# Kernel tuning notes

Measured on AMD Instinct MI355X. Metric: run time of the kernel, lower is better.

The kernel has to match this reference:

```python
import jax, jax.numpy as jnp
import numpy as np

N, E = 100000, 1600000
F_IN, H, HG, L, C = 128, 128, 128, 3, 40


def setup_inputs() -> dict:
    key = jax.random.key(0)
    ks = jax.random.split(key, 12)
    s = 0.05
    return dict(
        x=jax.random.normal(ks[0], (N, F_IN), jnp.float32),
        edge_index=jax.random.randint(ks[1], (2, E), 0, N),
        edge_weight=jax.random.uniform(ks[2], (E,), jnp.float32),
        h0=jax.random.normal(ks[3], (N, HG), jnp.float32),
        linW=jax.random.normal(ks[4], (F_IN, H), jnp.float32) * s,
        linB=jnp.zeros((H,), jnp.float32),
        convW=jax.random.normal(ks[5], (L, H, H), jnp.float32) * s,
        convB=jnp.zeros((L, H), jnp.float32),
        gru_Wih=jax.random.normal(ks[6], (3 * HG, H), jnp.float32) * s,
        gru_Whh=jax.random.normal(ks[7], (3 * HG, HG), jnp.float32) * s,
        gru_bih=jnp.zeros((3 * HG,), jnp.float32),
        gru_bhh=jnp.zeros((3 * HG,), jnp.float32),
        fcW=jax.random.normal(ks[8], (HG, C), jnp.float32) * s,
        fcB=jnp.zeros((C,), jnp.float32),
    )


def _gru(x, h, Wih, Whh, bih, bhh):
    # torch.nn.GRUCell math (gate order: r, z, n)
    gi = x @ Wih.T + bih  # [N, 3*HG]
    gh = h @ Whh.T + bhh  # [N, 3*HG]
    ir, iz, in_ = jnp.split(gi, 3, axis=-1)
    hr, hz, hn = jnp.split(gh, 3, axis=-1)
    r = jax.nn.sigmoid(ir + hr)
    z = jax.nn.sigmoid(iz + hz)
    n = jnp.tanh(in_ + r * hn)
    return (1.0 - z) * n + z * h


def _gcn_conv(x, src, dst, ew, W, b, n_nodes):
    # PyG GCNConv: linear -> symmetric-normalized sparse aggregation -> bias
    xw = x @ W  # [N, H]
    deg = jax.ops.segment_sum(ew, dst, num_segments=n_nodes)
    dinv = jnp.where(deg > 0, jax.lax.rsqrt(deg), 0.0)
    norm = dinv[src] * ew * dinv[dst]  # [E+N]
    msg = xw[src] * norm[:, None]      # gather + scale (irregular access)
    out = jax.ops.segment_sum(msg, dst, num_segments=n_nodes)  # scatter-add
    return out + b


def reference(x, edge_index, edge_weight, h0, linW, linB, convW, convB,
              gru_Wih, gru_Whh, gru_bih, gru_bhh, fcW, fcB):
    n_nodes = x.shape[0]
    # GCNConv default: add self-loops with weight 1 before normalization
    loops = jnp.arange(n_nodes)
    src = jnp.concatenate([edge_index[0], loops])
    dst = jnp.concatenate([edge_index[1], loops])
    ew = jnp.concatenate([edge_weight, jnp.ones((n_nodes,), edge_weight.dtype)])

    h = h0
    xh = jax.nn.relu(x @ linW + linB)
    h = _gru(xh, h, gru_Wih, gru_Whh, gru_bih, gru_bhh)
    for l in range(convW.shape[0]):  # fixed small layer count
        xh = jax.nn.relu(_gcn_conv(xh, src, dst, ew, convW[l], convB[l], n_nodes))
        h = _gru(xh, h, gru_Wih, gru_Whh, gru_bih, gru_bhh)
    return h @ fcW + fcB
```

## Files before the change

### kernel.cpp

```cpp
#include <hip/hip_runtime.h>
#include <hip/hip_bf16.h>
#include <math.h>

typedef __attribute__((ext_vector_type(8))) short bf8_t;
typedef __attribute__((ext_vector_type(4))) float f4_t;
typedef __attribute__((ext_vector_type(8))) unsigned short us8_t;

__device__ inline unsigned short f2bf(float f) {
  union { float f; unsigned u; } x; x.f = f;
  unsigned r = x.u + 0x7FFF + ((x.u >> 16) & 1);
  return (unsigned short)(r >> 16);
}
__device__ inline float bflo(unsigned v) {
  union { unsigned u; float f; } x; x.u = v << 16; return x.f;
}
__device__ inline float bfhi(unsigned v) {
  union { unsigned u; float f; } x; x.u = v & 0xFFFF0000u; return x.f;
}
__device__ inline float fast_sig(float x) {
  return __builtin_amdgcn_rcpf(1.f + __expf(-x));
}
__device__ inline float fast_tanh(float x) {
  return 1.f - 2.f * __builtin_amdgcn_rcpf(1.f + __expf(2.f * x));
}

__device__ inline void async_copy16(const void* g, void* l) {
  __builtin_amdgcn_global_load_lds(
      (const __attribute__((address_space(1))) unsigned int*)g,
      (__attribute__((address_space(3))) unsigned int*)l, 16, 0, 0);
}


__device__ inline void packB_body(const float* __restrict__ W,
                                  unsigned short* __restrict__ out,
                                  int K, int Ncols, int ldw, int trans, int bid) {
  int idx = bid * 256 + threadIdx.x;
  int total = (Ncols / 16) * (K / 32) * 64;
  if (idx >= total) return;
  int lane = idx & 63;
  int frag = idx >> 6;
  int kt = K / 32;
  int k0 = frag % kt;
  int n0 = frag / kt;
  int n = n0 * 16 + (lane & 15);
  int kbase = k0 * 32 + (lane >> 4) * 8;
  us8_t v;
#pragma unroll
  for (int j = 0; j < 8; ++j) {
    int k = kbase + j;
    float f = trans ? W[(size_t)n * ldw + k] : W[(size_t)k * ldw + n];
    v[j] = f2bf(f);
  }
  *(us8_t*)(out + (size_t)idx * 8) = v;
}

__device__ inline void gemm_body8(const unsigned short* __restrict__ A,
                                  const unsigned short* __restrict__ Bp,
                                  const float* __restrict__ bias,
                                  unsigned short* __restrict__ C, int M, int bid,
                                  bool relu, bool hasbias, unsigned char* smem) {
  int wave = threadIdx.x >> 6, lane = threadIdx.x & 63;
  int row0 = (bid * 8 + wave) * 16;
  int m = lane & 15, q = lane >> 4;

#pragma unroll
  for (int i = 0; i < 4; ++i) {
    int f = wave * 4 + i;
    async_copy16((const unsigned char*)Bp + (size_t)f * 1024 + lane * 16,
                 smem + f * 1024);
  }
  __syncthreads();
  if (row0 >= M) return;

  int arow = row0 + m; if (arow >= M) arow = M - 1;
  bf8_t a[4];
#pragma unroll
  for (int k0 = 0; k0 < 4; ++k0)
    a[k0] = *(const bf8_t*)(A + (size_t)arow * 128 + k0 * 32 + q * 8);

#pragma unroll
  for (int n0 = 0; n0 < 8; ++n0) {
    f4_t acc = {};
#pragma unroll
    for (int k0 = 0; k0 < 4; ++k0) {
      bf8_t b = *(const bf8_t*)(smem + (n0 * 4 + k0) * 1024 + lane * 16);
      acc = __builtin_amdgcn_mfma_f32_16x16x32_bf16(a[k0], b, acc, 0, 0, 0);
    }
    int col = n0 * 16 + m;
    float bs = hasbias ? bias[col] : 0.f;
#pragma unroll
    for (int r = 0; r < 4; ++r) {
      int grow = row0 + q * 4 + r;
      if (grow < M) {
        float v = acc[r] + bs;
        if (relu) v = fmaxf(v, 0.f);
        C[(size_t)grow * 128 + col] = f2bf(v);
      }
    }
  }
}

__device__ inline void gru_stage8(const unsigned short* __restrict__ Bi,
                                  const unsigned short* __restrict__ Bh,
                                  unsigned char* smem, int wave, int lane, int g) {
#pragma unroll
  for (int i = 0; i < 3; ++i) {
    int f = wave * 3 + i;
    int s = f >> 2, k0 = f & 3;
    int cc = g + 8 * (s >= 3 ? s - 3 : s);
    const unsigned short* src = (s < 3) ? Bi : Bh;
    async_copy16((const unsigned char*)src + ((size_t)(cc * 4 + k0)) * 1024 + lane * 16,
                 smem + f * 1024);
  }
}

__device__ inline void gru_core(const bf8_t* ax, const float* h_in, float* h_out,
                                const unsigned short* __restrict__ Bi,
                                const unsigned short* __restrict__ Bh,
                                const float* __restrict__ bih, const float* __restrict__ bhh,
                                int M, int row0, int wave, int lane, unsigned char* smem) {
  int m = lane & 15, q = lane >> 4;
  int arow = row0 + m; if (arow >= M) arow = M - 1;

  bf8_t ah[4];
#pragma unroll
  for (int k0 = 0; k0 < 4; ++k0) {
    const float* hp = h_in + (size_t)arow * 128 + k0 * 32 + q * 8;
    float4 h0 = *(const float4*)hp;
    float4 h1 = *(const float4*)(hp + 4);
    bf8_t t;
    t[0] = (short)f2bf(h0.x); t[1] = (short)f2bf(h0.y);
    t[2] = (short)f2bf(h0.z); t[3] = (short)f2bf(h0.w);
    t[4] = (short)f2bf(h1.x); t[5] = (short)f2bf(h1.y);
    t[6] = (short)f2bf(h1.z); t[7] = (short)f2bf(h1.w);
    ah[k0] = t;
  }

  int erow[4];
#pragma unroll
  for (int r = 0; r < 4; ++r) {
    int gr = row0 + q * 4 + r;
    erow[r] = (gr < M) ? gr : (M - 1);
  }

  float hp_cur[4], hp_nxt[4];
#pragma unroll
  for (int r = 0; r < 4; ++r)
    hp_cur[r] = h_in[(size_t)erow[r] * 128 + m];

#pragma unroll
  for (int g = 0; g < 8; ++g) {
    __syncthreads();
    f4_t air = {}, aiz = {}, ain = {}, ahr = {}, ahz = {}, ahn = {};
#pragma unroll
    for (int k0 = 0; k0 < 4; ++k0) {
      bf8_t br = *(const bf8_t*)(smem + (0 * 4 + k0) * 1024 + lane * 16);
      bf8_t bz = *(const bf8_t*)(smem + (1 * 4 + k0) * 1024 + lane * 16);
      bf8_t bn = *(const bf8_t*)(smem + (2 * 4 + k0) * 1024 + lane * 16);
      bf8_t cr = *(const bf8_t*)(smem + (3 * 4 + k0) * 1024 + lane * 16);
      bf8_t cz = *(const bf8_t*)(smem + (4 * 4 + k0) * 1024 + lane * 16);
      bf8_t cn = *(const bf8_t*)(smem + (5 * 4 + k0) * 1024 + lane * 16);
      air = __builtin_amdgcn_mfma_f32_16x16x32_bf16(ax[k0], br, air, 0, 0, 0);
      aiz = __builtin_amdgcn_mfma_f32_16x16x32_bf16(ax[k0], bz, aiz, 0, 0, 0);
      ain = __builtin_amdgcn_mfma_f32_16x16x32_bf16(ax[k0], bn, ain, 0, 0, 0);
      ahr = __builtin_amdgcn_mfma_f32_16x16x32_bf16(ah[k0], cr, ahr, 0, 0, 0);
      ahz = __builtin_amdgcn_mfma_f32_16x16x32_bf16(ah[k0], cz, ahz, 0, 0, 0);
      ahn = __builtin_amdgcn_mfma_f32_16x16x32_bf16(ah[k0], cn, ahn, 0, 0, 0);
    }
    if (g < 7) {
#pragma unroll
      for (int r = 0; r < 4; ++r)
        hp_nxt[r] = h_in[(size_t)erow[r] * 128 + (g + 1) * 16 + m];
    }
    __syncthreads();
    if (g < 7) gru_stage8(Bi, Bh, smem, wave, lane, g + 1);

    int col = g * 16 + m;
    float bir_ = bih[col], biz_ = bih[col + 128], bin_ = bih[col + 256];
    float bhr_ = bhh[col], bhz_ = bhh[col + 128], bhn_ = bhh[col + 256];
#pragma unroll
    for (int r = 0; r < 4; ++r) {
      int grow = row0 + q * 4 + r;
      if (grow < M) {
        float rr = fast_sig(air[r] + bir_ + ahr[r] + bhr_);
        float zz = fast_sig(aiz[r] + biz_ + ahz[r] + bhz_);
        float nn = fast_tanh(ain[r] + bin_ + rr * (ahn[r] + bhn_));
        h_out[(size_t)grow * 128 + col] = (1.f - zz) * nn + zz * hp_cur[r];
      }
    }
#pragma unroll
    for (int r = 0; r < 4; ++r) hp_cur[r] = hp_nxt[r];
  }
}


__global__ __launch_bounds__(256) void k_prep(
    const float* __restrict__ linW, const float* __restrict__ convW,
    const float* __restrict__ Wih, const float* __restrict__ Whh,
    unsigned short* __restrict__ linWp, unsigned short* __restrict__ convWp,
    unsigned short* __restrict__ Bi, unsigned short* __restrict__ Bh,
    int* __restrict__ cnt, int N) {
  int b = blockIdx.x;
  if (b < 8)  { packB_body(linW, linWp, 128, 128, 128, 0, b); return; }
  if (b < 32) { int l = (b - 8) >> 3;
                packB_body(convW + (size_t)l * 16384, convWp + (size_t)l * 16384,
                           128, 128, 128, 0, (b - 8) & 7); return; }
  if (b < 56) { packB_body(Wih, Bi, 128, 384, 128, 1, b - 32); return; }
  if (b < 80) { packB_body(Whh, Bh, 128, 384, 128, 1, b - 56); return; }
  int i = (b - 80) * 256 + threadIdx.x;
  if (i < N) cnt[i] = 0;
}

__global__ __launch_bounds__(256) void k_count_f2bf(
    const int* __restrict__ dst, int* __restrict__ cnt, int* __restrict__ pos, int E,
    const float* __restrict__ xin, unsigned short* __restrict__ xout, size_t n8,
    int nCnt) {
  if ((int)blockIdx.x < nCnt) {
    int e = blockIdx.x * 256 + threadIdx.x;
    if (e < E) pos[e] = atomicAdd(&cnt[dst[e]], 1);
    return;
  }
  size_t i = (size_t)(blockIdx.x - nCnt) * 256 + threadIdx.x;
  if (i >= n8) return;
  const float4* p = (const float4*)(xin + i * 8);
  float4 a = p[0], b = p[1];
  us8_t v;
  v[0] = f2bf(a.x); v[1] = f2bf(a.y); v[2] = f2bf(a.z); v[3] = f2bf(a.w);
  v[4] = f2bf(b.x); v[5] = f2bf(b.y); v[6] = f2bf(b.z); v[7] = f2bf(b.w);
  *(us8_t*)(xout + i * 8) = v;
}

__global__ __launch_bounds__(256) void k_scan_block(
    const int* __restrict__ cnt, int* __restrict__ partial,
    int* __restrict__ bsum, int n) {
  __shared__ int s[256];
  int tid = threadIdx.x;
  int i = blockIdx.x * 256 + tid;
  s[tid] = (i < n) ? cnt[i] : 0;
  __syncthreads();
#pragma unroll
  for (int d = 1; d < 256; d <<= 1) {
    int t = (tid >= d) ? s[tid - d] : 0;
    __syncthreads();
    s[tid] += t;
    __syncthreads();
  }
  if (i < n) partial[i] = s[tid];
  if (tid == 255) bsum[blockIdx.x] = s[255];
}

__global__ __launch_bounds__(512) void k_scan_sums(int* __restrict__ bsum, int nb) {
  __shared__ int s[512];
  int tid = threadIdx.x;
  s[tid] = (tid < nb) ? bsum[tid] : 0;
  __syncthreads();
#pragma unroll
  for (int d = 1; d < 512; d <<= 1) {
    int t = (tid >= d) ? s[tid - d] : 0;
    __syncthreads();
    s[tid] += t;
    __syncthreads();
  }
  if (tid < nb) bsum[tid] = s[tid];
}

__global__ __launch_bounds__(256) void k_scan_add(
    const int* __restrict__ partial, const int* __restrict__ bsum,
    int* __restrict__ rowptr, int n) {
  int i = blockIdx.x * 256 + threadIdx.x;
  if (i == 0) rowptr[0] = 0;
  if (i < n) {
    int v = partial[i] + (blockIdx.x > 0 ? bsum[blockIdx.x - 1] : 0);
    rowptr[i + 1] = v;
  }
}

__global__ __launch_bounds__(512) void k_fill(
    const int* __restrict__ src, const int* __restrict__ dst,
    const float* __restrict__ ew, const int* __restrict__ rowptr,
    const int* __restrict__ pos, int2* __restrict__ csr, int E) {
  int e = blockIdx.x * 512 + threadIdx.x;
  if (e >= E) return;
  int d = dst[e];
  int p = rowptr[d] + pos[e];
  unsigned long long v = (unsigned long long)(unsigned)src[e] |
                         ((unsigned long long)(unsigned)__float_as_int(ew[e]) << 32);
  __builtin_nontemporal_store(v, (unsigned long long*)(csr + p));
}

__global__ __launch_bounds__(512) void k_deg(
    const int* __restrict__ rowptr, const int2* __restrict__ csr,
    float* __restrict__ dinv, int N) {
  int n = blockIdx.x * 512 + threadIdx.x;
  if (n >= N) return;
  int b = rowptr[n], e = rowptr[n + 1];
  float s = 1.0f;
  for (int j = b; j < e; ++j) {
    unsigned long long v = __builtin_nontemporal_load((const unsigned long long*)(csr + j));
    s += __int_as_float((int)(v >> 32));
  }
  dinv[n] = rsqrtf(s);
}

__global__ __launch_bounds__(512) void k_norm(
    const int* __restrict__ rowptr, int2* __restrict__ csr,
    const float* __restrict__ dinv, int N) {
  int n = blockIdx.x * 512 + threadIdx.x;
  if (n >= N) return;
  int b = rowptr[n], e = rowptr[n + 1];
  float dn = dinv[n];
  for (int j = b; j < e; ++j) {
    unsigned long long v = __builtin_nontemporal_load((const unsigned long long*)(csr + j));
    int s = (int)v;
    float w = dinv[s] * __int_as_float((int)(v >> 32)) * dn;
    unsigned long long nv = (unsigned long long)(unsigned)s |
                            ((unsigned long long)(unsigned)__float_as_int(w) << 32);
    __builtin_nontemporal_store(nv, (unsigned long long*)(csr + j));
  }
}

template<bool RELU, bool BIAS>
__global__ __launch_bounds__(512, 4) void k_gemm(
    const unsigned short* __restrict__ A, const unsigned short* __restrict__ Bp,
    const float* __restrict__ bias, unsigned short* __restrict__ C, int M) {
  __shared__ unsigned char smem[32 * 1024];
  gemm_body8(A, Bp, bias, C, M, blockIdx.x, RELU, BIAS, smem);
}

__global__ __launch_bounds__(512, 4) void k_gru(
    const unsigned short* __restrict__ xh, const float* h_in, float* h_out,
    const unsigned short* __restrict__ Bi, const unsigned short* __restrict__ Bh,
    const float* __restrict__ bih, const float* __restrict__ bhh, int M) {
  __shared__ unsigned char smem[24 * 1024];
  int wave = threadIdx.x >> 6, lane = threadIdx.x & 63;
  int row0 = (blockIdx.x * 8 + wave) * 16;
  gru_stage8(Bi, Bh, smem, wave, lane, 0);
  int m = lane & 15, q = lane >> 4;
  int arow = row0 + m; if (arow >= M) arow = M - 1;
  bf8_t ax[4];
#pragma unroll
  for (int k0 = 0; k0 < 4; ++k0)
    ax[k0] = *(const bf8_t*)(xh + (size_t)arow * 128 + k0 * 32 + q * 8);
  gru_core(ax, h_in, h_out, Bi, Bh, bih, bhh, M, row0, wave, lane, smem);
}


__global__ __launch_bounds__(256) void k_gather(
    const int* __restrict__ rowptr, const int2* __restrict__ csr,
    const unsigned* __restrict__ xw,
    const float* __restrict__ dinv, const float* __restrict__ bias,
    unsigned* __restrict__ out, int N) {
  int wave = threadIdx.x >> 6;
  int lane = threadIdx.x & 63;
  int node = __builtin_amdgcn_readfirstlane(blockIdx.x * 4 + wave);
  if (node >= N) return;
  int beg = __builtin_amdgcn_readfirstlane(rowptr[node]);
  int end = __builtin_amdgcn_readfirstlane(rowptr[node + 1]);

  float accl = 0.f, acch = 0.f;
  int k = beg;
  for (; k + 4 <= end; k += 4) {
    unsigned long long r0 = __builtin_nontemporal_load((const unsigned long long*)(csr + k));
    unsigned long long r1 = __builtin_nontemporal_load((const unsigned long long*)(csr + k + 1));
    unsigned long long r2 = __builtin_nontemporal_load((const unsigned long long*)(csr + k + 2));
    unsigned long long r3 = __builtin_nontemporal_load((const unsigned long long*)(csr + k + 3));
    unsigned v0 = xw[((size_t)(unsigned)r0 << 6) + lane];
    unsigned v1 = xw[((size_t)(unsigned)r1 << 6) + lane];
    unsigned v2 = xw[((size_t)(unsigned)r2 << 6) + lane];
    unsigned v3 = xw[((size_t)(unsigned)r3 << 6) + lane];
    float w0 = __int_as_float((int)(r0 >> 32)), w1 = __int_as_float((int)(r1 >> 32));
    float w2 = __int_as_float((int)(r2 >> 32)), w3 = __int_as_float((int)(r3 >> 32));
    accl += bflo(v0) * w0; acch += bfhi(v0) * w0;
    accl += bflo(v1) * w1; acch += bfhi(v1) * w1;
    accl += bflo(v2) * w2; acch += bfhi(v2) * w2;
    accl += bflo(v3) * w3; acch += bfhi(v3) * w3;
  }
  for (; k < end; ++k) {
    unsigned long long r = __builtin_nontemporal_load((const unsigned long long*)(csr + k));
    unsigned v = xw[((size_t)(unsigned)r << 6) + lane];
    float w = __int_as_float((int)(r >> 32));
    accl += bflo(v) * w; acch += bfhi(v) * w;
  }

  float di = dinv[node];
  float sn = di * di;
  unsigned vs = xw[((size_t)node << 6) + lane];
  float2 b = *(const float2*)(bias + lane * 2);
  float rl = fmaxf(accl + bflo(vs) * sn + b.x, 0.f);
  float rh = fmaxf(acch + bfhi(vs) * sn + b.y, 0.f);
  unsigned o = (unsigned)f2bf(rl) | ((unsigned)f2bf(rh) << 16);
  out[((size_t)node << 6) + lane] = o;
}


template<bool RELU, bool BIAS>
__global__ __launch_bounds__(256) void k_gemm128(
    const float* __restrict__ A, const float* __restrict__ B,
    const float* __restrict__ bias, float* __restrict__ C, int M, int Nc) {
  __shared__ float As[64][36];
  __shared__ float Bs[32][64];
  int tid = threadIdx.x;
  int tx = tid & 15, ty = tid >> 4;
  int row0 = blockIdx.y * 64, col0 = blockIdx.x * 64;
  float acc[4][4] = {};

  for (int k0 = 0; k0 < 128; k0 += 32) {
#pragma unroll
    for (int i = 0; i < 2; ++i) {
      int f = tid + i * 256;
      int r = f >> 3, c4 = f & 7;
      int gr = row0 + r;
      float4 v = make_float4(0.f, 0.f, 0.f, 0.f);
      if (gr < M) v = *(const float4*)(A + (size_t)gr * 128 + k0 + c4 * 4);
      *(float4*)(&As[r][c4 * 4]) = v;
    }
#pragma unroll
    for (int i = 0; i < 2; ++i) {
      int f = tid + i * 256;
      int r = f >> 4, c4 = f & 15;
      int gc = col0 + c4 * 4;
      float4 v = make_float4(0.f, 0.f, 0.f, 0.f);
      if (gc + 3 < Nc) v = *(const float4*)(B + (size_t)(k0 + r) * Nc + gc);
      *(float4*)(&Bs[r][c4 * 4]) = v;
    }
    __syncthreads();
#pragma unroll
    for (int kk = 0; kk < 32; ++kk) {
      float4 b = *(float4*)(&Bs[kk][tx * 4]);
      float a0 = As[ty * 4 + 0][kk];
      float a1 = As[ty * 4 + 1][kk];
      float a2 = As[ty * 4 + 2][kk];
      float a3 = As[ty * 4 + 3][kk];
      acc[0][0] += a0 * b.x; acc[0][1] += a0 * b.y; acc[0][2] += a0 * b.z; acc[0][3] += a0 * b.w;
      acc[1][0] += a1 * b.x; acc[1][1] += a1 * b.y; acc[1][2] += a1 * b.z; acc[1][3] += a1 * b.w;
      acc[2][0] += a2 * b.x; acc[2][1] += a2 * b.y; acc[2][2] += a2 * b.z; acc[2][3] += a2 * b.w;
      acc[3][0] += a3 * b.x; acc[3][1] += a3 * b.y; acc[3][2] += a3 * b.z; acc[3][3] += a3 * b.w;
    }
    __syncthreads();
  }

#pragma unroll
  for (int i = 0; i < 4; ++i) {
    int gr = row0 + ty * 4 + i;
    if (gr >= M) continue;
#pragma unroll
    for (int j = 0; j < 4; ++j) {
      int gc = col0 + tx * 4 + j;
      if (gc >= Nc) continue;
      float v = acc[i][j];
      if (BIAS) v += bias[gc];
      if (RELU) v = fmaxf(v, 0.f);
      C[(size_t)gr * Nc + gc] = v;
    }
  }
}


extern "C" void kernel_launch(void* const* d_in, const int* in_sizes, int n_in,
                              void* d_out, int out_size, void* d_ws, size_t ws_size,
                              hipStream_t stream) {
  const float* x    = (const float*)d_in[0];
  const int*   ei   = (const int*)d_in[1];
  const float* ew   = (const float*)d_in[2];
  const float* h0   = (const float*)d_in[3];
  const float* linW = (const float*)d_in[4];
  const float* linB = (const float*)d_in[5];
  const float* convW= (const float*)d_in[6];
  const float* convB= (const float*)d_in[7];
  const float* Wih  = (const float*)d_in[8];
  const float* Whh  = (const float*)d_in[9];
  const float* bih  = (const float*)d_in[10];
  const float* bhh  = (const float*)d_in[11];
  const float* fcW  = (const float*)d_in[12];
  const float* fcB  = (const float*)d_in[13];

  int N = in_sizes[0] / 128;
  int E = in_sizes[1] / 2;
  const int* srcI = ei;
  const int* dstI = ei + E;
  int nb = (N + 255) / 256;

  float* ws = (float*)d_ws;
  size_t off = 0;
  float* dinv = ws + off; off += (size_t)N;
  if (off & 1) off++;
  float* h    = ws + off; off += (size_t)N * 128;
  int* iws = (int*)(ws + off);
  size_t ioff = 0;
  int2* csr    = (int2*)iws; ioff += (size_t)2 * E;
  int* cnt     = iws + ioff; ioff += (size_t)N;
  int* partial = iws + ioff; ioff += (size_t)N;
  int* bsum    = iws + ioff; ioff += 512;
  int* rowptr  = iws + ioff; ioff += (size_t)N + 1;
  ioff = (ioff + 3) & ~(size_t)3;
  unsigned short* usws = (unsigned short*)(iws + ioff);
  size_t uoff = 0;
  unsigned short* x_bf   = usws + uoff; uoff += (size_t)N * 128;
  unsigned short* xh_bf  = usws + uoff; uoff += (size_t)N * 128;
  unsigned short* xw_bf  = usws + uoff; uoff += (size_t)N * 128;
  unsigned short* linWp  = usws + uoff; uoff += 128 * 128;
  unsigned short* convWp = usws + uoff; uoff += 3 * 128 * 128;
  unsigned short* Bi     = usws + uoff; uoff += 384 * 128;
  unsigned short* Bh     = usws + uoff; uoff += 384 * 128;

  int* pos = (int*)xw_bf;

  int gw8  = (N + 127) / 128;
  int nCnt = (E + 255) / 256;
  int nF2  = (int)(((size_t)N * 16 + 255) / 256);
  int n512 = (N + 511) / 512;
  int e512 = (E + 511) / 512;
  int ggat = (N + 3) / 4;

  k_prep<<<80 + nb, 256, 0, stream>>>(linW, convW, Wih, Whh,
                                      linWp, convWp, Bi, Bh, cnt, N);
  k_count_f2bf<<<nCnt + nF2, 256, 0, stream>>>(dstI, cnt, pos, E,
                                               x, x_bf, (size_t)N * 16, nCnt);
  k_scan_block<<<nb, 256, 0, stream>>>(cnt, partial, bsum, N);
  k_scan_sums<<<1, 512, 0, stream>>>(bsum, nb);
  k_scan_add<<<nb, 256, 0, stream>>>(partial, bsum, rowptr, N);
  k_fill<<<e512, 512, 0, stream>>>(srcI, dstI, ew, rowptr, pos, csr, E);
  k_deg<<<n512, 512, 0, stream>>>(rowptr, csr, dinv, N);
  k_norm<<<n512, 512, 0, stream>>>(rowptr, csr, dinv, N);
  k_gemm<true, true><<<gw8, 512, 0, stream>>>(x_bf, linWp, linB, xh_bf, N);
  k_gru<<<gw8, 512, 0, stream>>>(xh_bf, h0, h, Bi, Bh, bih, bhh, N);
  for (int l = 0; l < 3; ++l) {
    k_gemm<false, false><<<gw8, 512, 0, stream>>>(
        xh_bf, convWp + (size_t)l * 128 * 128, nullptr, xw_bf, N);
    k_gather<<<ggat, 256, 0, stream>>>(
        rowptr, csr, (const unsigned*)xw_bf, dinv, convB + (size_t)l * 128,
        (unsigned*)xh_bf, N);
    k_gru<<<gw8, 512, 0, stream>>>(xh_bf, h, h, Bi, Bh, bih, bhh, N);
  }
  dim3 g40(1, (N + 63) / 64);
  k_gemm128<false, true><<<g40, 256, 0, stream>>>(h, fcW, fcB, (float*)d_out, N, 40);
}
```

Before: 982.3 us.

## Fuse input linear into count kernel, double-buffer GRU weights, shrink blocks to 4 waves

The separate fp32-to-bf16 conversion pass and the input linear GEMM are merged: the linear layer now reads fp32 x directly and packs to bf16 in registers, and it runs inside the edge-count kernel launch. The GRU kernel double-buffers its per-column-group weight tiles in LDS, so the next group's async loads overlap the current MFMAs and one barrier per iteration is dropped. Blocks shrink from 8 to 4 waves, so each block stages more weight fragments per wave and uses twice the LDS in GRU, which may lower occupancy.

```diff
diff --git a/kernel.cpp b/kernel.cpp
--- a/kernel.cpp
+++ b/kernel.cpp
@@ -28,6 +28,17 @@
   __builtin_amdgcn_global_load_lds(
       (const __attribute__((address_space(1))) unsigned int*)g,
       (__attribute__((address_space(3))) unsigned int*)l, 16, 0, 0);
+}
+
+__device__ inline bf8_t pack_bf8(const float* p) {
+  float4 a = *(const float4*)p;
+  float4 b = *(const float4*)(p + 4);
+  bf8_t t;
+  t[0] = (short)f2bf(a.x); t[1] = (short)f2bf(a.y);
+  t[2] = (short)f2bf(a.z); t[3] = (short)f2bf(a.w);
+  t[4] = (short)f2bf(b.x); t[5] = (short)f2bf(b.y);
+  t[6] = (short)f2bf(b.z); t[7] = (short)f2bf(b.w);
+  return t;
 }
 
 
@@ -54,18 +65,19 @@
   *(us8_t*)(out + (size_t)idx * 8) = v;
 }
 
-__device__ inline void gemm_body8(const unsigned short* __restrict__ A,
+template<bool RELU, bool BIAS, bool F32A>
+__device__ inline void gemm_body4(const void* __restrict__ Araw,
                                   const unsigned short* __restrict__ Bp,
                                   const float* __restrict__ bias,
                                   unsigned short* __restrict__ C, int M, int bid,
-                                  bool relu, bool hasbias, unsigned char* smem) {
+                                  unsigned char* smem) {
   int wave = threadIdx.x >> 6, lane = threadIdx.x & 63;
-  int row0 = (bid * 8 + wave) * 16;
+  int row0 = (bid * 4 + wave) * 16;
   int m = lane & 15, q = lane >> 4;
 
 #pragma unroll
-  for (int i = 0; i < 4; ++i) {
-    int f = wave * 4 + i;
+  for (int i = 0; i < 8; ++i) {
+    int f = wave * 8 + i;
     async_copy16((const unsigned char*)Bp + (size_t)f * 1024 + lane * 16,
                  smem + f * 1024);
   }
@@ -75,8 +87,14 @@
   int arow = row0 + m; if (arow >= M) arow = M - 1;
   bf8_t a[4];
 #pragma unroll
-  for (int k0 = 0; k0 < 4; ++k0)
-    a[k0] = *(const bf8_t*)(A + (size_t)arow * 128 + k0 * 32 + q * 8);
+  for (int k0 = 0; k0 < 4; ++k0) {
+    if (F32A) {
+      a[k0] = pack_bf8((const float*)Araw + (size_t)arow * 128 + k0 * 32 + q * 8);
+    } else {
+      a[k0] = *(const bf8_t*)((const unsigned short*)Araw +
+                              (size_t)arow * 128 + k0 * 32 + q * 8);
+    }
+  }
 
 #pragma unroll
   for (int n0 = 0; n0 < 8; ++n0) {
@@ -87,54 +105,45 @@
       acc = __builtin_amdgcn_mfma_f32_16x16x32_bf16(a[k0], b, acc, 0, 0, 0);
     }
     int col = n0 * 16 + m;
-    float bs = hasbias ? bias[col] : 0.f;
+    float bs = BIAS ? bias[col] : 0.f;
 #pragma unroll
     for (int r = 0; r < 4; ++r) {
       int grow = row0 + q * 4 + r;
       if (grow < M) {
         float v = acc[r] + bs;
-        if (relu) v = fmaxf(v, 0.f);
+        if (RELU) v = fmaxf(v, 0.f);
         C[(size_t)grow * 128 + col] = f2bf(v);
       }
     }
   }
 }
 
-__device__ inline void gru_stage8(const unsigned short* __restrict__ Bi,
+__device__ inline void gru_stage4(const unsigned short* __restrict__ Bi,
                                   const unsigned short* __restrict__ Bh,
-                                  unsigned char* smem, int wave, int lane, int g) {
-#pragma unroll
-  for (int i = 0; i < 3; ++i) {
-    int f = wave * 3 + i;
-    int s = f >> 2, k0 = f & 3;
+                                  unsigned char* half, int wave, int lane, int g) {
+#pragma unroll
+  for (int s = 0; s < 6; ++s) {
     int cc = g + 8 * (s >= 3 ? s - 3 : s);
     const unsigned short* src = (s < 3) ? Bi : Bh;
-    async_copy16((const unsigned char*)src + ((size_t)(cc * 4 + k0)) * 1024 + lane * 16,
-                 smem + f * 1024);
-  }
-}
-
-__device__ inline void gru_core(const bf8_t* ax, const float* h_in, float* h_out,
-                                const unsigned short* __restrict__ Bi,
-                                const unsigned short* __restrict__ Bh,
-                                const float* __restrict__ bih, const float* __restrict__ bhh,
-                                int M, int row0, int wave, int lane, unsigned char* smem) {
+    int f = s * 4 + wave;
+    async_copy16((const unsigned char*)src + ((size_t)(cc * 4 + wave)) * 1024 + lane * 16,
+                 half + f * 1024);
+  }
+}
+
+__device__ inline void gru_core4(const bf8_t* ax, const float* h_in, float* h_out,
+                                 const unsigned short* __restrict__ Bi,
+                                 const unsigned short* __restrict__ Bh,
+                                 const float* __restrict__ bih, const float* __restrict__ bhh,
+                                 int M, int row0, int wave, int lane,
+                                 unsigned char* smem) {
   int m = lane & 15, q = lane >> 4;
   int arow = row0 + m; if (arow >= M) arow = M - 1;
 
   bf8_t ah[4];
 #pragma unroll
-  for (int k0 = 0; k0 < 4; ++k0) {
-    const float* hp = h_in + (size_t)arow * 128 + k0 * 32 + q * 8;
-    float4 h0 = *(const float4*)hp;
-    float4 h1 = *(const float4*)(hp + 4);
-    bf8_t t;
-    t[0] = (short)f2bf(h0.x); t[1] = (short)f2bf(h0.y);
-    t[2] = (short)f2bf(h0.z); t[3] = (short)f2bf(h0.w);
-    t[4] = (short)f2bf(h1.x); t[5] = (short)f2bf(h1.y);
-    t[6] = (short)f2bf(h1.z); t[7] = (short)f2bf(h1.w);
-    ah[k0] = t;
-  }
+  for (int k0 = 0; k0 < 4; ++k0)
+    ah[k0] = pack_bf8(h_in + (size_t)arow * 128 + k0 * 32 + q * 8);
 
   int erow[4];
 #pragma unroll
@@ -151,15 +160,19 @@
 #pragma unroll
   for (int g = 0; g < 8; ++g) {
     __syncthreads();
+    if (g < 7)
+      gru_stage4(Bi, Bh, smem + ((g + 1) & 1) * (24 * 1024), wave, lane, g + 1);
+    unsigned char* cur = smem + (g & 1) * (24 * 1024);
+
     f4_t air = {}, aiz = {}, ain = {}, ahr = {}, ahz = {}, ahn = {};
 #pragma unroll
     for (int k0 = 0; k0 < 4; ++k0) {
-      bf8_t br = *(const bf8_t*)(smem + (0 * 4 + k0) * 1024 + lane * 16);
-      bf8_t bz = *(const bf8_t*)(smem + (1 * 4 + k0) * 1024 + lane * 16);
-      bf8_t bn = *(const bf8_t*)(smem + (2 * 4 + k0) * 1024 + lane * 16);
-      bf8_t cr = *(const bf8_t*)(smem + (3 * 4 + k0) * 1024 + lane * 16);
-      bf8_t cz = *(const bf8_t*)(smem + (4 * 4 + k0) * 1024 + lane * 16);
-      bf8_t cn = *(const bf8_t*)(smem + (5 * 4 + k0) * 1024 + lane * 16);
+      bf8_t br = *(const bf8_t*)(cur + (0 * 4 + k0) * 1024 + lane * 16);
+      bf8_t bz = *(const bf8_t*)(cur + (1 * 4 + k0) * 1024 + lane * 16);
+      bf8_t bn = *(const bf8_t*)(cur + (2 * 4 + k0) * 1024 + lane * 16);
+      bf8_t cr = *(const bf8_t*)(cur + (3 * 4 + k0) * 1024 + lane * 16);
+      bf8_t cz = *(const bf8_t*)(cur + (4 * 4 + k0) * 1024 + lane * 16);
+      bf8_t cn = *(const bf8_t*)(cur + (5 * 4 + k0) * 1024 + lane * 16);
       air = __builtin_amdgcn_mfma_f32_16x16x32_bf16(ax[k0], br, air, 0, 0, 0);
       aiz = __builtin_amdgcn_mfma_f32_16x16x32_bf16(ax[k0], bz, aiz, 0, 0, 0);
       ain = __builtin_amdgcn_mfma_f32_16x16x32_bf16(ax[k0], bn, ain, 0, 0, 0);
@@ -172,8 +185,6 @@
       for (int r = 0; r < 4; ++r)
         hp_nxt[r] = h_in[(size_t)erow[r] * 128 + (g + 1) * 16 + m];
     }
-    __syncthreads();
-    if (g < 7) gru_stage8(Bi, Bh, smem, wave, lane, g + 1);
 
     int col = g * 16 + m;
     float bir_ = bih[col], biz_ = bih[col + 128], bin_ = bih[col + 256];
@@ -211,23 +222,18 @@
   if (i < N) cnt[i] = 0;
 }
 
-__global__ __launch_bounds__(256) void k_count_f2bf(
+__global__ __launch_bounds__(256) void k_count_lin(
     const int* __restrict__ dst, int* __restrict__ cnt, int* __restrict__ pos, int E,
-    const float* __restrict__ xin, unsigned short* __restrict__ xout, size_t n8,
+    const float* __restrict__ x, const unsigned short* __restrict__ linWp,
+    const float* __restrict__ linB, unsigned short* __restrict__ xh, int M,
     int nCnt) {
+  __shared__ unsigned char smem[32 * 1024];
   if ((int)blockIdx.x < nCnt) {
     int e = blockIdx.x * 256 + threadIdx.x;
     if (e < E) pos[e] = atomicAdd(&cnt[dst[e]], 1);
     return;
   }
-  size_t i = (size_t)(blockIdx.x - nCnt) * 256 + threadIdx.x;
-  if (i >= n8) return;
-  const float4* p = (const float4*)(xin + i * 8);
-  float4 a = p[0], b = p[1];
-  us8_t v;
-  v[0] = f2bf(a.x); v[1] = f2bf(a.y); v[2] = f2bf(a.z); v[3] = f2bf(a.w);
-  v[4] = f2bf(b.x); v[5] = f2bf(b.y); v[6] = f2bf(b.z); v[7] = f2bf(b.w);
-  *(us8_t*)(xout + i * 8) = v;
+  gemm_body4<true, true, true>(x, linWp, linB, xh, M, blockIdx.x - nCnt, smem);
 }
 
 __global__ __launch_bounds__(256) void k_scan_block(
@@ -319,29 +325,28 @@
   }
 }
 
-template<bool RELU, bool BIAS>
-__global__ __launch_bounds__(512, 4) void k_gemm(
+__global__ __launch_bounds__(256) void k_conv(
     const unsigned short* __restrict__ A, const unsigned short* __restrict__ Bp,
-    const float* __restrict__ bias, unsigned short* __restrict__ C, int M) {
+    unsigned short* __restrict__ C, int M) {
   __shared__ unsigned char smem[32 * 1024];
-  gemm_body8(A, Bp, bias, C, M, blockIdx.x, RELU, BIAS, smem);
-}
-
-__global__ __launch_bounds__(512, 4) void k_gru(
+  gemm_body4<false, false, false>(A, Bp, nullptr, C, M, blockIdx.x, smem);
+}
+
+__global__ __launch_bounds__(256, 3) void k_gru(
     const unsigned short* __restrict__ xh, const float* h_in, float* h_out,
     const unsigned short* __restrict__ Bi, const unsigned short* __restrict__ Bh,
     const float* __restrict__ bih, const float* __restrict__ bhh, int M) {
-  __shared__ unsigned char smem[24 * 1024];
+  __shared__ unsigned char smem[2 * 24 * 1024];
   int wave = threadIdx.x >> 6, lane = threadIdx.x & 63;
-  int row0 = (blockIdx.x * 8 + wave) * 16;
-  gru_stage8(Bi, Bh, smem, wave, lane, 0);
+  int row0 = (blockIdx.x * 4 + wave) * 16;
+  gru_stage4(Bi, Bh, smem, wave, lane, 0);
   int m = lane & 15, q = lane >> 4;
   int arow = row0 + m; if (arow >= M) arow = M - 1;
   bf8_t ax[4];
 #pragma unroll
   for (int k0 = 0; k0 < 4; ++k0)
     ax[k0] = *(const bf8_t*)(xh + (size_t)arow * 128 + k0 * 32 + q * 8);
-  gru_core(ax, h_in, h_out, Bi, Bh, bih, bhh, M, row0, wave, lane, smem);
+  gru_core4(ax, h_in, h_out, Bi, Bh, bih, bhh, M, row0, wave, lane, smem);
 }
 
 
@@ -495,7 +500,6 @@
   ioff = (ioff + 3) & ~(size_t)3;
   unsigned short* usws = (unsigned short*)(iws + ioff);
   size_t uoff = 0;
-  unsigned short* x_bf   = usws + uoff; uoff += (size_t)N * 128;
   unsigned short* xh_bf  = usws + uoff; uoff += (size_t)N * 128;
   unsigned short* xw_bf  = usws + uoff; uoff += (size_t)N * 128;
   unsigned short* linWp  = usws + uoff; uoff += 128 * 128;
@@ -505,32 +509,30 @@
 
   int* pos = (int*)xw_bf;
 
-  int gw8  = (N + 127) / 128;
+  int gw4  = (N + 63) / 64;
   int nCnt = (E + 255) / 256;
-  int nF2  = (int)(((size_t)N * 16 + 255) / 256);
   int n512 = (N + 511) / 512;
   int e512 = (E + 511) / 512;
   int ggat = (N + 3) / 4;
 
   k_prep<<<80 + nb, 256, 0, stream>>>(linW, convW, Wih, Whh,
                                       linWp, convWp, Bi, Bh, cnt, N);
-  k_count_f2bf<<<nCnt + nF2, 256, 0, stream>>>(dstI, cnt, pos, E,
-                                               x, x_bf, (size_t)N * 16, nCnt);
+  k_count_lin<<<nCnt + gw4, 256, 0, stream>>>(dstI, cnt, pos, E,
+                                              x, linWp, linB, xh_bf, N, nCnt);
   k_scan_block<<<nb, 256, 0, stream>>>(cnt, partial, bsum, N);
   k_scan_sums<<<1, 512, 0, stream>>>(bsum, nb);
   k_scan_add<<<nb, 256, 0, stream>>>(partial, bsum, rowptr, N);
   k_fill<<<e512, 512, 0, stream>>>(srcI, dstI, ew, rowptr, pos, csr, E);
   k_deg<<<n512, 512, 0, stream>>>(rowptr, csr, dinv, N);
   k_norm<<<n512, 512, 0, stream>>>(rowptr, csr, dinv, N);
-  k_gemm<true, true><<<gw8, 512, 0, stream>>>(x_bf, linWp, linB, xh_bf, N);
-  k_gru<<<gw8, 512, 0, stream>>>(xh_bf, h0, h, Bi, Bh, bih, bhh, N);
+  k_gru<<<gw4, 256, 0, stream>>>(xh_bf, h0, h, Bi, Bh, bih, bhh, N);
   for (int l = 0; l < 3; ++l) {
-    k_gemm<false, false><<<gw8, 512, 0, stream>>>(
-        xh_bf, convWp + (size_t)l * 128 * 128, nullptr, xw_bf, N);
+    k_conv<<<gw4, 256, 0, stream>>>(
+        xh_bf, convWp + (size_t)l * 128 * 128, xw_bf, N);
     k_gather<<<ggat, 256, 0, stream>>>(
         rowptr, csr, (const unsigned*)xw_bf, dinv, convB + (size_t)l * 128,
         (unsigned*)xh_bf, N);
-    k_gru<<<gw8, 512, 0, stream>>>(xh_bf, h, h, Bi, Bh, bih, bhh, N);
+    k_gru<<<gw4, 256, 0, stream>>>(xh_bf, h, h, Bi, Bh, bih, bhh, N);
   }
   dim3 g40(1, (N + 63) / 64);
   k_gemm128<false, true><<<g40, 256, 0, stream>>>(h, fcW, fcB, (float*)d_out, N, 40);
```

After: 888.2 us. 1.11x faster.
